# Kernel optimization log

Measured on AMD Instinct MI355X. Metric: run time of the kernel, lower is better.

## Reference

```python
import jax, jax.numpy as jnp
import numpy as np

NUM_ITERS = 20  # fixed in the original forward: transcribe(dna, iterations=20)


def transcribe(dna_seed, dna_a, dna_b):
    """Fractal DNA decompression: 20 elementwise contractive-map iterations
    over the full weight tensor, starting from the DNA seed."""
    def step(w, ab):
        a, b = ab
        w = a * w + b * jnp.sin(w)
        return w, None
    w, _ = jax.lax.scan(step, dna_seed, (dna_a, dna_b))
    return w  # [out_features, in_features]


def setup_inputs() -> dict:
    key = jax.random.key(0)
    k1, k2, k3, k4, k5 = jax.random.split(key, 5)
    TOKENS, IN_F, OUT_F = 2048, 4096, 4096
    return {
        "x": jax.random.normal(k1, (TOKENS, IN_F), dtype=jnp.float32),
        "dna_seed": jax.random.normal(k2, (OUT_F, IN_F), dtype=jnp.float32),
        "dna_a": jax.random.uniform(k3, (NUM_ITERS,), dtype=jnp.float32),
        "dna_b": jax.random.uniform(k4, (NUM_ITERS,), dtype=jnp.float32),
        "bias": jax.random.normal(k5, (OUT_F,), dtype=jnp.float32),
    }


def reference(x, dna_seed, dna_a, dna_b, bias):
    weight = transcribe(dna_seed, dna_a, dna_b)          # [out, in]
    # F.linear(x, weight, bias) == x @ weight.T + bias
    return jnp.einsum('ti,oi->to', x, weight) + bias     # [tokens, out]
```

## Files before the change

### kernel.cpp

```cpp
#include <hip/hip_runtime.h>
#include <hip/hip_bf16.h>

typedef __attribute__((ext_vector_type(8))) short short8;
typedef __attribute__((ext_vector_type(4))) float floatx4;

#define TOKENS 2048
#define IN_F   4096
#define OUT_F  4096
#define NITER  20

__device__ __forceinline__ unsigned short f2bf(float f) {
    unsigned int u = __builtin_bit_cast(unsigned int, f);
    u += 0x7fffu + ((u >> 16) & 1u);
    return (unsigned short)(u >> 16);
}

template <int ITERS>
__global__ __launch_bounds__(256) void transcribe_kernel(
    const float4* __restrict__ in,
    const float* __restrict__ da, const float* __restrict__ db,
    ushort* __restrict__ out, int nvec)
{
    int i = blockIdx.x * 256 + threadIdx.x;
    if (i >= nvec) return;
    float4 w = in[i];
#pragma unroll
    for (int t = 0; t < ITERS; t++) {
        float a = da[t], b = db[t];
        w.x = a * w.x + b * __sinf(w.x);
        w.y = a * w.y + b * __sinf(w.y);
        w.z = a * w.z + b * __sinf(w.z);
        w.w = a * w.w + b * __sinf(w.w);
    }
    ushort4 o;
    o.x = f2bf(w.x); o.y = f2bf(w.y); o.z = f2bf(w.z); o.w = f2bf(w.w);
    *(ushort4*)(out + 4 * (size_t)i) = o;
}

__device__ __forceinline__ void g2l16(const ushort* g, ushort* l) {
    __builtin_amdgcn_global_load_lds(
        (const __attribute__((address_space(1))) unsigned int*)g,
        (__attribute__((address_space(3))) unsigned int*)l, 16, 0, 0);
}

__global__ __launch_bounds__(256) void gemm_bt_kernel(
    const ushort* __restrict__ A,
    const ushort* __restrict__ B,
    const float* __restrict__ bias,
    float* __restrict__ C,
    int M, int N, int K)
{
    __shared__ ushort As[128 * 32];
    __shared__ ushort Bs[128 * 32];

    const int tid  = threadIdx.x;
    const int lane = tid & 63;
    const int wid  = tid >> 6;
    const int bn   = blockIdx.x;
    const int bm   = blockIdx.y;
    const int wm   = (wid >> 1) << 6;
    const int wn   = (wid & 1) << 6;
    const int fm   = lane & 15;
    const int fk   = (lane >> 4) << 3;

    const int row0 = tid >> 2;
    const int seg  = (tid & 3) << 3;

    const ushort* gA = A + (size_t)(bm * 128) * K;
    const ushort* gB = B + (size_t)(bn * 128) * K;

    floatx4 acc[4][4];
#pragma unroll
    for (int i = 0; i < 4; i++)
#pragma unroll
        for (int j = 0; j < 4; j++)
            acc[i][j] = (floatx4){0.f, 0.f, 0.f, 0.f};

    for (int k0 = 0; k0 < K; k0 += 32) {
        g2l16(gA + (size_t)row0 * K + k0 + seg,        As + row0 * 32 + seg);
        g2l16(gA + (size_t)(row0 + 64) * K + k0 + seg, As + (row0 + 64) * 32 + seg);
        g2l16(gB + (size_t)row0 * K + k0 + seg,        Bs + row0 * 32 + seg);
        g2l16(gB + (size_t)(row0 + 64) * K + k0 + seg, Bs + (row0 + 64) * 32 + seg);
        __syncthreads();

        short8 af[4], bfr[4];
#pragma unroll
        for (int i = 0; i < 4; i++)
            af[i] = *(const short8*)(As + (wm + i * 16 + fm) * 32 + fk);
#pragma unroll
        for (int j = 0; j < 4; j++)
            bfr[j] = *(const short8*)(Bs + (wn + j * 16 + fm) * 32 + fk);
#pragma unroll
        for (int i = 0; i < 4; i++)
#pragma unroll
            for (int j = 0; j < 4; j++)
                acc[i][j] = __builtin_amdgcn_mfma_f32_16x16x32_bf16(
                    af[i], bfr[j], acc[i][j], 0, 0, 0);
        __syncthreads();
    }

    const int cn = lane & 15;
    const int cm = (lane >> 4) << 2;
    float bv[4];
#pragma unroll
    for (int j = 0; j < 4; j++)
        bv[j] = bias[bn * 128 + wn + j * 16 + cn];
#pragma unroll
    for (int i = 0; i < 4; i++) {
#pragma unroll
        for (int r = 0; r < 4; r++) {
            int m = bm * 128 + wm + i * 16 + cm + r;
            float* crow = C + (size_t)m * N + bn * 128 + wn + cn;
#pragma unroll
            for (int j = 0; j < 4; j++)
                crow[j * 16] = acc[i][j][r] + bv[j];
        }
    }
}

extern "C" void kernel_launch(void* const* d_in, const int* in_sizes, int n_in,
                              void* d_out, int out_size, void* d_ws, size_t ws_size,
                              hipStream_t stream) {
    const float* x    = (const float*)d_in[0];
    const float* seed = (const float*)d_in[1];
    const float* da   = (const float*)d_in[2];
    const float* db   = (const float*)d_in[3];
    const float* bias = (const float*)d_in[4];
    float* out        = (float*)d_out;

    ushort* w_bf = (ushort*)d_ws;
    ushort* x_bf = w_bf + (size_t)OUT_F * IN_F;

    const int nvec_w = OUT_F * IN_F / 4;
    const int nvec_x = TOKENS * IN_F / 4;

    transcribe_kernel<NITER><<<nvec_w / 256, 256, 0, stream>>>(
        (const float4*)seed, da, db, w_bf, nvec_w);
    transcribe_kernel<0><<<nvec_x / 256, 256, 0, stream>>>(
        (const float4*)x, da, db, x_bf, nvec_x);

    dim3 grid(OUT_F / 128, TOKENS / 128);
    gemm_bt_kernel<<<grid, 256, 0, stream>>>(x_bf, w_bf, bias, out,
                                             TOKENS, OUT_F, IN_F);
}
```

Baseline: 253.6 us.

## Swizzle GEMM LDS tile layout and use hardware sine in transcribe

Applies an XOR swizzle to the 16-byte k-segments of the A/B LDS tiles. Since global_load_lds fixes each lane's LDS destination, the swizzle is applied to the global source address instead, and the fragment reads use the matching permutation. The aim is to remove LDS bank conflicts on the MFMA fragment loads. Separately, the transcribe loop now calls the hardware v_sin instruction with a 1/(2π) prescale instead of __sinf, which cuts instruction count per iteration but may lose accuracy for large arguments.

Result: no change. 249.3 us (-1.7%).

```diff
diff --git a/kernel.cpp b/kernel.cpp
--- a/kernel.cpp
+++ b/kernel.cpp
@@ -9,10 +9,16 @@
 #define OUT_F  4096
 #define NITER  20
 
+#define INV_2PI 0.15915494309189535f
+
 __device__ __forceinline__ unsigned short f2bf(float f) {
     unsigned int u = __builtin_bit_cast(unsigned int, f);
     u += 0x7fffu + ((u >> 16) & 1u);
     return (unsigned short)(u >> 16);
+}
+
+__device__ __forceinline__ float hw_sin(float x) {
+    return __builtin_amdgcn_sinf(x * INV_2PI);
 }
 
 template <int ITERS>
@@ -27,10 +33,10 @@
 #pragma unroll
     for (int t = 0; t < ITERS; t++) {
         float a = da[t], b = db[t];
-        w.x = a * w.x + b * __sinf(w.x);
-        w.y = a * w.y + b * __sinf(w.y);
-        w.z = a * w.z + b * __sinf(w.z);
-        w.w = a * w.w + b * __sinf(w.w);
+        w.x = a * w.x + b * hw_sin(w.x);
+        w.y = a * w.y + b * hw_sin(w.y);
+        w.z = a * w.z + b * hw_sin(w.z);
+        w.w = a * w.w + b * hw_sin(w.w);
     }
     ushort4 o;
     o.x = f2bf(w.x); o.y = f2bf(w.y); o.z = f2bf(w.z); o.w = f2bf(w.w);
@@ -61,10 +67,12 @@
     const int wm   = (wid >> 1) << 6;
     const int wn   = (wid & 1) << 6;
     const int fm   = lane & 15;
-    const int fk   = (lane >> 4) << 3;
+    const int fkd  = (((lane >> 4) ^ ((fm >> 1) & 3)) << 3);
 
     const int row0 = tid >> 2;
-    const int seg  = (tid & 3) << 3;
+    const int psg  = tid & 3;
+    const int gsg  = (psg ^ ((row0 >> 1) & 3)) << 3;
+    const int lsg  = psg << 3;
 
     const ushort* gA = A + (size_t)(bm * 128) * K;
     const ushort* gB = B + (size_t)(bn * 128) * K;
@@ -77,19 +85,19 @@
             acc[i][j] = (floatx4){0.f, 0.f, 0.f, 0.f};
 
     for (int k0 = 0; k0 < K; k0 += 32) {
-        g2l16(gA + (size_t)row0 * K + k0 + seg,        As + row0 * 32 + seg);
-        g2l16(gA + (size_t)(row0 + 64) * K + k0 + seg, As + (row0 + 64) * 32 + seg);
-        g2l16(gB + (size_t)row0 * K + k0 + seg,        Bs + row0 * 32 + seg);
-        g2l16(gB + (size_t)(row0 + 64) * K + k0 + seg, Bs + (row0 + 64) * 32 + seg);
+        g2l16(gA + (size_t)row0 * K + k0 + gsg,        As + row0 * 32 + lsg);
+        g2l16(gA + (size_t)(row0 + 64) * K + k0 + gsg, As + (row0 + 64) * 32 + lsg);
+        g2l16(gB + (size_t)row0 * K + k0 + gsg,        Bs + row0 * 32 + lsg);
+        g2l16(gB + (size_t)(row0 + 64) * K + k0 + gsg, Bs + (row0 + 64) * 32 + lsg);
         __syncthreads();
 
         short8 af[4], bfr[4];
 #pragma unroll
         for (int i = 0; i < 4; i++)
-            af[i] = *(const short8*)(As + (wm + i * 16 + fm) * 32 + fk);
+            af[i] = *(const short8*)(As + (wm + i * 16 + fm) * 32 + fkd);
 #pragma unroll
         for (int j = 0; j < 4; j++)
-            bfr[j] = *(const short8*)(Bs + (wn + j * 16 + fm) * 32 + fk);
+            bfr[j] = *(const short8*)(Bs + (wn + j * 16 + fm) * 32 + fkd);
 #pragma unroll
         for (int i = 0; i < 4; i++)
 #pragma unroll
```
